# Kernel tuning notes

Measured on AMD Instinct MI355X. Metric: run time of the kernel, lower is better.

## Reference

```python
import jax, jax.numpy as jnp
import numpy as np

H = 12          # num_attention_heads
D = 64          # num_embed_hidden == attention_head_size
B, T = 4, 2048
SCALE = 1.0 / np.sqrt(D)


def setup_inputs() -> dict:
    key = jax.random.key(0)
    ks = jax.random.split(key, 7)
    P = H * D  # num_attn_proj = 768
    s = 1.0 / np.sqrt(D)
    return {
        "hidden_states": jax.random.normal(ks[0], (B, T, D), dtype=jnp.float32),
        "attention_mask": jnp.ones((B, T), dtype=jnp.float32),
        "Wq": jax.random.normal(ks[1], (D, P), dtype=jnp.float32) * s,
        "bq": jnp.zeros((P,), dtype=jnp.float32),
        "Wk": jax.random.normal(ks[2], (D, P), dtype=jnp.float32) * s,
        "bk": jnp.zeros((P,), dtype=jnp.float32),
        "Wv": jax.random.normal(ks[3], (D, P), dtype=jnp.float32) * s,
        "bv": jnp.zeros((P,), dtype=jnp.float32),
    }


def reference(hidden_states, attention_mask, Wq, bq, Wk, bk, Wv, bv):
    b, t, _ = hidden_states.shape
    # QKV projections -> [B, H, T, D]
    def proj(W, bias):
        return (hidden_states @ W + bias).reshape(b, t, H, D).transpose(0, 2, 1, 3)
    q = proj(Wq, bq)
    k = proj(Wk, bk)
    v = proj(Wv, bv)
    # [B, H, T, T] scores
    scores = jnp.einsum("bhqd,bhkd->bhqk", q, k) * SCALE
    mask = (1.0 - attention_mask)[:, None, None, :] * -10000.0
    scores = scores + mask
    attn = jax.nn.softmax(scores, axis=-1)
    # dropout is identity in eval mode
    y = jnp.einsum("bhqk,bhkd->bhqd", attn, v)
    return y.transpose(0, 2, 1, 3).reshape(b, t, H * D)
```

## Files before the change

kernel.cpp:

```cpp
#include <hip/hip_runtime.h>
#include <hip/hip_bf16.h>

#define NH 12
#define HD 64
#define NB 4
#define SEQ 2048
#define NP 768
#define LOG2E 1.44269504f
#define MASK_L2 14426.9504f

typedef __bf16 bf16x8 __attribute__((ext_vector_type(8)));
typedef __bf16 bf16x2 __attribute__((ext_vector_type(2)));
typedef float f32x2 __attribute__((ext_vector_type(2)));
typedef float f32x4 __attribute__((ext_vector_type(4)));
typedef float f32x16 __attribute__((ext_vector_type(16)));
typedef unsigned u32x4 __attribute__((ext_vector_type(4)));

static __device__ __forceinline__ bf16x8 load_bf16x8(const __bf16* p) {
    return *reinterpret_cast<const bf16x8*>(p);
}
static __device__ __forceinline__ float hw_exp2(float x) {
    return __builtin_amdgcn_exp2f(x);
}
static __device__ __forceinline__ unsigned cvtpk2(float lo, float hi) {
    f32x2 t; t[0] = lo; t[1] = hi;
    return __builtin_bit_cast(unsigned, __builtin_convertvector(t, bf16x2));
}
static __device__ __forceinline__ void async16(const __bf16* g, __bf16* l) {
    __builtin_amdgcn_global_load_lds(
        (const __attribute__((address_space(1))) unsigned*)(g),
        (__attribute__((address_space(3))) unsigned*)(l), 16, 0, 0);
}

__global__ __launch_bounds__(256) void qkv_kernel(
    const float* __restrict__ hidden,
    const float* __restrict__ Wq, const float* __restrict__ Wk,
    const float* __restrict__ Wv,
    const float* __restrict__ bq, const float* __restrict__ bk,
    const float* __restrict__ bv,
    __bf16* __restrict__ Qw, __bf16* __restrict__ Kf, __bf16* __restrict__ Vf)
{
    __shared__ __bf16 wtileT[64][72];
    __shared__ __bf16 ot[64][72];

    const int tid  = threadIdx.x;
    const int lane = tid & 63;
    const int w    = tid >> 6;
    const int g    = lane >> 4;
    const int n    = lane & 15;
    const int n32  = lane & 31;
    const int hi   = lane >> 5;

    const int row0 = blockIdx.x * 64;
    const int gi   = blockIdx.y;
    const int b_   = row0 >> 11;
    const int t0   = row0 & (SEQ - 1);
    const int kb64 = t0 >> 6;

    const float* hrow = hidden + (size_t)(row0 + w * 16 + n) * HD + 8 * g;
    f32x4 h0 = *(const f32x4*)(hrow);
    f32x4 h1 = *(const f32x4*)(hrow + 4);
    f32x4 h2 = *(const f32x4*)(hrow + 32);
    f32x4 h3 = *(const f32x4*)(hrow + 36);
    bf16x8 a0, a1;
    #pragma unroll
    for (int j = 0; j < 4; ++j) {
        a0[j]     = (__bf16)h0[j];
        a0[j + 4] = (__bf16)h1[j];
        a1[j]     = (__bf16)h2[j];
        a1[j + 4] = (__bf16)h3[j];
    }

    const int dr   = tid >> 2;
    const int coff = (tid & 3) * 16;

    for (int tt = 0; tt < 6; ++tt) {
        const int tile_id = gi * 6 + tt;
        const int proj    = tile_id / 12;
        const int head    = tile_id % 12;
        const int bh      = b_ * NH + head;
        const float* W    = proj == 0 ? Wq : (proj == 1 ? Wk : Wv);
        const float* bias = proj == 0 ? bq : (proj == 1 ? bk : bv);
        const float qs    = (proj == 0) ? 0.125f * LOG2E : 1.0f;

        const float* wr = W + (size_t)dr * NP + head * 64 + coff;
        f32x4 x0 = *(const f32x4*)(wr);
        f32x4 x1 = *(const f32x4*)(wr + 4);
        f32x4 x2 = *(const f32x4*)(wr + 8);
        f32x4 x3 = *(const f32x4*)(wr + 12);
        #pragma unroll
        for (int i = 0; i < 4; ++i) {
            wtileT[coff + i     ][dr] = (__bf16)(x0[i] * qs);
            wtileT[coff + 4 + i ][dr] = (__bf16)(x1[i] * qs);
            wtileT[coff + 8 + i ][dr] = (__bf16)(x2[i] * qs);
            wtileT[coff + 12 + i][dr] = (__bf16)(x3[i] * qs);
        }
        __syncthreads();

        #pragma unroll
        for (int dt = 0; dt < 4; ++dt) {
            const bf16x8 b0 = *(const bf16x8*)&wtileT[dt * 16 + n][8 * g];
            const bf16x8 b1 = *(const bf16x8*)&wtileT[dt * 16 + n][32 + 8 * g];
            f32x4 acc = {0.f, 0.f, 0.f, 0.f};
            acc = __builtin_amdgcn_mfma_f32_16x16x32_bf16(a0, b0, acc, 0, 0, 0);
            acc = __builtin_amdgcn_mfma_f32_16x16x32_bf16(a1, b1, acc, 0, 0, 0);
            const float bb = bias[head * 64 + dt * 16 + n] * qs;
            #pragma unroll
            for (int r = 0; r < 4; ++r)
                ot[w * 16 + 4 * g + r][dt * 16 + n] = (__bf16)(acc[r] + bb);
        }
        __syncthreads();

        if (proj == 0) {
            __bf16* dst = Qw + ((size_t)bh * SEQ + t0 + w * 16) * HD;
            const int tr = lane >> 2;
            const int d0 = (lane & 3) * 16;
            *(bf16x8*)(dst + (size_t)tr * HD + d0)     = *(const bf16x8*)&ot[w * 16 + tr][d0];
            *(bf16x8*)(dst + (size_t)tr * HD + d0 + 8) = *(const bf16x8*)&ot[w * 16 + tr][d0 + 8];
        } else if (proj == 1) {
            __bf16* base = Kf + (size_t)bh * SEQ * HD + (size_t)kb64 * 4096;
            #pragma unroll
            for (int sub = 0; sub < 2; ++sub) {
                const bf16x8 fr = *(const bf16x8*)&ot[sub * 32 + n32][w * 16 + 8 * hi];
                *(bf16x8*)(base + (size_t)(w * 2 + sub) * 512 + lane * 8) = fr;
            }
        } else {
            __bf16* base = Vf + (size_t)bh * SEQ * HD + (size_t)kb64 * 4096;
            #pragma unroll
            for (int dsub = 0; dsub < 2; ++dsub) {
                bf16x8 v;
                #pragma unroll
                for (int j = 0; j < 8; ++j)
                    v[j] = ot[w * 16 + ((j & 3) + 8 * (j >> 2) + 4 * hi)][dsub * 32 + n32];
                *(bf16x8*)(base + (size_t)(w * 2 + dsub) * 512 + lane * 8) = v;
            }
        }
    }
}

__global__ __launch_bounds__(256, 3) void flash_attn_kernel(
    const __bf16* __restrict__ Qw, const __bf16* __restrict__ Kf,
    const __bf16* __restrict__ Vf, const float* __restrict__ amask,
    float* __restrict__ out)
{
    __shared__ __align__(16) union {
        __bf16 kv[2][8192];
        float  et[4][32][68];
    } u;
    __shared__ __bf16 mdd[SEQ];

    const int tid  = threadIdx.x;
    const int lane = tid & 63;
    const int w    = tid >> 6;
    const int n32  = lane & 31;
    const int hi   = lane >> 5;

    const int bid  = blockIdx.x;
    const int xcd  = bid & 7;
    const int slot = bid >> 3;
    const int bh   = xcd * 6 + (slot >> 4);
    const int qblk = slot & 15;
    const int b_   = bh / NH;
    const int h    = bh % NH;
    const int q0   = qblk * 128 + w * 32;

    const float* mp = amask + (size_t)b_ * SEQ;
    #pragma unroll
    for (int i = 0; i < 8; ++i) {
        const int idx = w * 512 + i * 64 + lane;
        mdd[idx] = (__bf16)fmaf(mp[idx], MASK_L2, -MASK_L2);
    }

    const __bf16* Qrow = Qw + ((size_t)bh * SEQ + q0 + n32) * HD + 8 * hi;
    bf16x8 qf[4];
    #pragma unroll
    for (int d = 0; d < 4; ++d) qf[d] = load_bf16x8(Qrow + d * 16);

    bf16x8 qone;
    #pragma unroll
    for (int j = 0; j < 8; ++j) qone[j] = (__bf16)0.0f;
    if (hi == 0) qone[0] = (__bf16)1.0f;

    const size_t bhoff = (size_t)bh * SEQ * HD;
    const __bf16* gbase = (w < 2 ? Kf : Vf) + bhoff + (w & 1) * 2048 + (size_t)lane * 8;
    __bf16* const lbase = &u.kv[0][0] + ((w & 2) ? 4096 : 0) + (w & 1) * 2048;

    #pragma unroll
    for (int c = 0; c < 4; ++c) async16(gbase + c * 512, lbase + c * 512);
    __syncthreads();

    f32x16 o0 = {0,0,0,0,0,0,0,0,0,0,0,0,0,0,0,0};
    f32x16 o1 = {0,0,0,0,0,0,0,0,0,0,0,0,0,0,0,0};
    f32x2 lsl2 = {0.f, 0.f};

    for (int it = 0; it < 32; ++it) {
        const int cur = it & 1;
        const int kb  = it << 6;

        {
            const __bf16* s = gbase + (size_t)((it + 1) & 31) * 4096;
            __bf16* dl = lbase + (cur ^ 1) * 8192;
            #pragma unroll
            for (int c = 0; c < 4; ++c) async16(s + c * 512, dl + c * 512);
        }

        const __bf16* Kb = &u.kv[cur][0];
        const __bf16* Vb = Kb + 4096;

        bf16x8 kca[4], kcb[4];
        #pragma unroll
        for (int d = 0; d < 4; ++d) {
            kca[d] = load_bf16x8(Kb + (2 * d) * 512 + lane * 8);
            kcb[d] = load_bf16x8(Kb + (2 * d + 1) * 512 + lane * 8);
        }

        bf16x8 maa, mab;
        #pragma unroll
        for (int j = 0; j < 8; ++j) { maa[j] = (__bf16)0.0f; mab[j] = (__bf16)0.0f; }
        maa[0] = mdd[kb + n32];
        mab[0] = mdd[kb + 32 + n32];

        f32x16 sa = {0,0,0,0,0,0,0,0,0,0,0,0,0,0,0,0};
        f32x16 sb = {0,0,0,0,0,0,0,0,0,0,0,0,0,0,0,0};
        __builtin_amdgcn_s_setprio(1);
        #pragma unroll
        for (int d = 0; d < 4; ++d)
            sa = __builtin_amdgcn_mfma_f32_32x32x16_bf16(kca[d], qf[d], sa, 0, 0, 0);
        sa = __builtin_amdgcn_mfma_f32_32x32x16_bf16(maa, qone, sa, 0, 0, 0);
        #pragma unroll
        for (int d = 0; d < 4; ++d)
            sb = __builtin_amdgcn_mfma_f32_32x32x16_bf16(kcb[d], qf[d], sb, 0, 0, 0);
        sb = __builtin_amdgcn_mfma_f32_32x32x16_bf16(mab, qone, sb, 0, 0, 0);
        __builtin_amdgcn_s_setprio(0);

        bf16x8 vf0[4], vf1[4];
        #pragma unroll
        for (int c = 0; c < 4; ++c) {
            vf0[c] = load_bf16x8(Vb + (2 * c) * 512 + lane * 8);
            vf1[c] = load_bf16x8(Vb + (2 * c + 1) * 512 + lane * 8);
        }

        bf16x8 P0, P1;
        {
            float p[16];
            #pragma unroll
            for (int r = 0; r < 16; ++r) p[r] = hw_exp2(sa[r]);
            u32x4 B0, B1;
            #pragma unroll
            for (int i = 0; i < 4; ++i) {
                B0[i] = cvtpk2(p[2 * i],     p[2 * i + 1]);
                B1[i] = cvtpk2(p[8 + 2 * i], p[8 + 2 * i + 1]);
            }
            #pragma unroll
            for (int i = 0; i < 8; ++i) {
                f32x2 t; t[0] = p[2 * i]; t[1] = p[2 * i + 1];
                lsl2 += t;
            }
            P0 = __builtin_bit_cast(bf16x8, B0);
            P1 = __builtin_bit_cast(bf16x8, B1);
        }
        __builtin_amdgcn_s_setprio(1);
        o0 = __builtin_amdgcn_mfma_f32_32x32x16_bf16(vf0[0], P0, o0, 0, 0, 0);
        o1 = __builtin_amdgcn_mfma_f32_32x32x16_bf16(vf1[0], P0, o1, 0, 0, 0);
        o0 = __builtin_amdgcn_mfma_f32_32x32x16_bf16(vf0[1], P1, o0, 0, 0, 0);
        o1 = __builtin_amdgcn_mfma_f32_32x32x16_bf16(vf1[1], P1, o1, 0, 0, 0);
        __builtin_amdgcn_s_setprio(0);

        bf16x8 P2, P3;
        {
            float p[16];
            #pragma unroll
            for (int r = 0; r < 16; ++r) p[r] = hw_exp2(sb[r]);
            u32x4 B0, B1;
            #pragma unroll
            for (int i = 0; i < 4; ++i) {
                B0[i] = cvtpk2(p[2 * i],     p[2 * i + 1]);
                B1[i] = cvtpk2(p[8 + 2 * i], p[8 + 2 * i + 1]);
            }
            #pragma unroll
            for (int i = 0; i < 8; ++i) {
                f32x2 t; t[0] = p[2 * i]; t[1] = p[2 * i + 1];
                lsl2 += t;
            }
            P2 = __builtin_bit_cast(bf16x8, B0);
            P3 = __builtin_bit_cast(bf16x8, B1);
        }
        __builtin_amdgcn_s_setprio(1);
        o0 = __builtin_amdgcn_mfma_f32_32x32x16_bf16(vf0[2], P2, o0, 0, 0, 0);
        o1 = __builtin_amdgcn_mfma_f32_32x32x16_bf16(vf1[2], P2, o1, 0, 0, 0);
        o0 = __builtin_amdgcn_mfma_f32_32x32x16_bf16(vf0[3], P3, o0, 0, 0, 0);
        o1 = __builtin_amdgcn_mfma_f32_32x32x16_bf16(vf1[3], P3, o1, 0, 0, 0);
        __builtin_amdgcn_s_setprio(0);

        __syncthreads();
    }

    float rs = lsl2[0] + lsl2[1];
    rs += __shfl_xor(rs, 32);

    #pragma unroll
    for (int k = 0; k < 4; ++k) {
        f32x4 t0, t1;
        #pragma unroll
        for (int j = 0; j < 4; ++j) { t0[j] = o0[4 * k + j]; t1[j] = o1[4 * k + j]; }
        *(f32x4*)&u.et[w][n32][8 * k + 4 * hi]      = t0;
        *(f32x4*)&u.et[w][n32][32 + 8 * k + 4 * hi] = t1;
    }
    const int d0 = (lane & 7) * 8;
    #pragma unroll
    for (int pass = 0; pass < 4; ++pass) {
        const int q = pass * 8 + (lane >> 3);
        const float linv = 1.0f / __shfl(rs, q);
        const float* er = &u.et[w][q][d0];
        f32x4 r0 = *(const f32x4*)(er);
        f32x4 r1 = *(const f32x4*)(er + 4);
        #pragma unroll
        for (int i = 0; i < 4; ++i) { r0[i] *= linv; r1[i] *= linv; }
        float* orow = out + ((size_t)b_ * SEQ + q0 + q) * NP + h * HD + d0;
        *(f32x4*)(orow)     = r0;
        *(f32x4*)(orow + 4) = r1;
    }
}

extern "C" void kernel_launch(void* const* d_in, const int* in_sizes, int n_in,
                              void* d_out, int out_size, void* d_ws, size_t ws_size,
                              hipStream_t stream) {
    const float* hidden = (const float*)d_in[0];
    const float* amask  = (const float*)d_in[1];
    const float* Wq     = (const float*)d_in[2];
    const float* bq     = (const float*)d_in[3];
    const float* Wk     = (const float*)d_in[4];
    const float* bk     = (const float*)d_in[5];
    const float* Wv     = (const float*)d_in[6];
    const float* bv     = (const float*)d_in[7];
    float* out = (float*)d_out;

    const size_t elems = (size_t)NB * NH * SEQ * HD;
    __bf16* Qw = (__bf16*)d_ws;
    __bf16* Kf = Qw + elems;
    __bf16* Vf = Kf + elems;

    qkv_kernel<<<dim3(128, 6), 256, 0, stream>>>(
        hidden, Wq, Wk, Wv, bq, bk, bv, Qw, Kf, Vf);

    flash_attn_kernel<<<dim3(768), 256, 0, stream>>>(
        Qw, Kf, Vf, amask, out);
}
```

Baseline: 158.9 us.

## Software-pipeline QK^T of next tile with PV of previous tile using triple-buffered V

Restructures the flash-attention main loop so each iteration computes the QK^T scores for tile t while doing exp and PV for tile t-1, with K double-buffered and V triple-buffered in LDS. The loop is manually unrolled by two through a templated body, with a prologue and an epilogue for the final PV. The aim is to overlap MFMA score work with the exp/convert VALU work and V loads, hiding latency within a wave. The cost is more live accumulator registers (two sets of scores), extra LDS for the third V buffer, and more complex control flow, which could hurt occupancy at three blocks per CU.

```diff
diff --git a/kernel.cpp b/kernel.cpp
--- a/kernel.cpp
+++ b/kernel.cpp
@@ -138,15 +138,127 @@
     }
 }
 
+struct KVbuf {
+    __bf16 k[2][4096];
+    __bf16 v[3][4096];
+};
+
+union FlashLds {
+    KVbuf s;
+    float et[4][32][68];
+};
+
+static __device__ __forceinline__ int rot3(int x) { return x + 1 == 3 ? 0 : x + 1; }
+
+template<int KS, bool STG, bool DOPV>
+static __device__ __forceinline__ void fbody(
+    int t, int vprev, int vnext, int w, int lane, int n32,
+    FlashLds* u, const __bf16* mdd, const __bf16* gsrc,
+    const bf16x8 (&qf)[4], const bf16x8& qone,
+    f32x16& sap, f32x16& sbp, f32x16& san, f32x16& sbn,
+    f32x16& o0, f32x16& o1, f32x2& lsl2)
+{
+    if (STG) {
+        __bf16* dst = (w < 2) ? &u->s.k[KS ^ 1][0] + (w & 1) * 2048
+                              : &u->s.v[vnext][0] + (w & 1) * 2048;
+        const __bf16* src = gsrc + (size_t)(t + 1) * 4096;
+        #pragma unroll
+        for (int c = 0; c < 4; ++c) async16(src + c * 512, dst + c * 512);
+    }
+
+    const __bf16* Kb = &u->s.k[KS][0];
+    bf16x8 kca[4], kcb[4];
+    #pragma unroll
+    for (int d = 0; d < 4; ++d) {
+        kca[d] = load_bf16x8(Kb + (2 * d) * 512 + lane * 8);
+        kcb[d] = load_bf16x8(Kb + (2 * d + 1) * 512 + lane * 8);
+    }
+    const int kb = t << 6;
+    bf16x8 maa, mab;
+    #pragma unroll
+    for (int j = 0; j < 8; ++j) { maa[j] = (__bf16)0.0f; mab[j] = (__bf16)0.0f; }
+    maa[0] = mdd[kb + n32];
+    mab[0] = mdd[kb + 32 + n32];
+
+    f32x16 z = {0,0,0,0,0,0,0,0,0,0,0,0,0,0,0,0};
+    san = z; sbn = z;
+    __builtin_amdgcn_s_setprio(1);
+    #pragma unroll
+    for (int d = 0; d < 4; ++d)
+        san = __builtin_amdgcn_mfma_f32_32x32x16_bf16(kca[d], qf[d], san, 0, 0, 0);
+    san = __builtin_amdgcn_mfma_f32_32x32x16_bf16(maa, qone, san, 0, 0, 0);
+    #pragma unroll
+    for (int d = 0; d < 4; ++d)
+        sbn = __builtin_amdgcn_mfma_f32_32x32x16_bf16(kcb[d], qf[d], sbn, 0, 0, 0);
+    sbn = __builtin_amdgcn_mfma_f32_32x32x16_bf16(mab, qone, sbn, 0, 0, 0);
+    __builtin_amdgcn_s_setprio(0);
+
+    if (DOPV) {
+        const __bf16* Vb = &u->s.v[vprev][0];
+        bf16x8 P0, P1;
+        {
+            u32x4 B0, B1;
+            #pragma unroll
+            for (int i = 0; i < 4; ++i) {
+                float e0 = hw_exp2(sap[2 * i]),     e1 = hw_exp2(sap[2 * i + 1]);
+                float f0 = hw_exp2(sap[8 + 2 * i]), f1 = hw_exp2(sap[8 + 2 * i + 1]);
+                B0[i] = cvtpk2(e0, e1);
+                B1[i] = cvtpk2(f0, f1);
+                f32x2 acc; acc[0] = e0 + f0; acc[1] = e1 + f1;
+                lsl2 += acc;
+            }
+            P0 = __builtin_bit_cast(bf16x8, B0);
+            P1 = __builtin_bit_cast(bf16x8, B1);
+        }
+        {
+            bf16x8 v0 = load_bf16x8(Vb + 0 * 512 + lane * 8);
+            bf16x8 v1 = load_bf16x8(Vb + 1 * 512 + lane * 8);
+            bf16x8 v2 = load_bf16x8(Vb + 2 * 512 + lane * 8);
+            bf16x8 v3 = load_bf16x8(Vb + 3 * 512 + lane * 8);
+            __builtin_amdgcn_s_setprio(1);
+            o0 = __builtin_amdgcn_mfma_f32_32x32x16_bf16(v0, P0, o0, 0, 0, 0);
+            o1 = __builtin_amdgcn_mfma_f32_32x32x16_bf16(v1, P0, o1, 0, 0, 0);
+            o0 = __builtin_amdgcn_mfma_f32_32x32x16_bf16(v2, P1, o0, 0, 0, 0);
+            o1 = __builtin_amdgcn_mfma_f32_32x32x16_bf16(v3, P1, o1, 0, 0, 0);
+            __builtin_amdgcn_s_setprio(0);
+        }
+        bf16x8 P2, P3;
+        {
+            u32x4 B0, B1;
+            #pragma unroll
+            for (int i = 0; i < 4; ++i) {
+                float e0 = hw_exp2(sbp[2 * i]),     e1 = hw_exp2(sbp[2 * i + 1]);
+                float f0 = hw_exp2(sbp[8 + 2 * i]), f1 = hw_exp2(sbp[8 + 2 * i + 1]);
+                B0[i] = cvtpk2(e0, e1);
+                B1[i] = cvtpk2(f0, f1);
+                f32x2 acc; acc[0] = e0 + f0; acc[1] = e1 + f1;
+                lsl2 += acc;
+            }
+            P2 = __builtin_bit_cast(bf16x8, B0);
+            P3 = __builtin_bit_cast(bf16x8, B1);
+        }
+        {
+            bf16x8 v4 = load_bf16x8(Vb + 4 * 512 + lane * 8);
+            bf16x8 v5 = load_bf16x8(Vb + 5 * 512 + lane * 8);
+            bf16x8 v6 = load_bf16x8(Vb + 6 * 512 + lane * 8);
+            bf16x8 v7 = load_bf16x8(Vb + 7 * 512 + lane * 8);
+            __builtin_amdgcn_s_setprio(1);
+            o0 = __builtin_amdgcn_mfma_f32_32x32x16_bf16(v4, P2, o0, 0, 0, 0);
+            o1 = __builtin_amdgcn_mfma_f32_32x32x16_bf16(v5, P2, o1, 0, 0, 0);
+            o0 = __builtin_amdgcn_mfma_f32_32x32x16_bf16(v6, P3, o0, 0, 0, 0);
+            o1 = __builtin_amdgcn_mfma_f32_32x32x16_bf16(v7, P3, o1, 0, 0, 0);
+            __builtin_amdgcn_s_setprio(0);
+        }
+    }
+    __syncthreads();
+}
+
 __global__ __launch_bounds__(256, 3) void flash_attn_kernel(
     const __bf16* __restrict__ Qw, const __bf16* __restrict__ Kf,
     const __bf16* __restrict__ Vf, const float* __restrict__ amask,
     float* __restrict__ out)
 {
-    __shared__ __align__(16) union {
-        __bf16 kv[2][8192];
-        float  et[4][32][68];
-    } u;
+    __shared__ __align__(16) FlashLds u;
     __shared__ __bf16 mdd[SEQ];
 
     const int tid  = threadIdx.x;
@@ -182,121 +294,81 @@
     if (hi == 0) qone[0] = (__bf16)1.0f;
 
     const size_t bhoff = (size_t)bh * SEQ * HD;
-    const __bf16* gbase = (w < 2 ? Kf : Vf) + bhoff + (w & 1) * 2048 + (size_t)lane * 8;
-    __bf16* const lbase = &u.kv[0][0] + ((w & 2) ? 4096 : 0) + (w & 1) * 2048;
-
-    #pragma unroll
-    for (int c = 0; c < 4; ++c) async16(gbase + c * 512, lbase + c * 512);
+    const __bf16* gsrc = (w < 2 ? Kf : Vf) + bhoff + (w & 1) * 2048 + (size_t)lane * 8;
+
+    {
+        __bf16* dst = (w < 2) ? &u.s.k[0][0] + (w & 1) * 2048
+                              : &u.s.v[0][0] + (w & 1) * 2048;
+        #pragma unroll
+        for (int c = 0; c < 4; ++c) async16(gsrc + c * 512, dst + c * 512);
+    }
     __syncthreads();
 
     f32x16 o0 = {0,0,0,0,0,0,0,0,0,0,0,0,0,0,0,0};
     f32x16 o1 = {0,0,0,0,0,0,0,0,0,0,0,0,0,0,0,0};
     f32x2 lsl2 = {0.f, 0.f};
-
-    for (int it = 0; it < 32; ++it) {
-        const int cur = it & 1;
-        const int kb  = it << 6;
-
-        {
-            const __bf16* s = gbase + (size_t)((it + 1) & 31) * 4096;
-            __bf16* dl = lbase + (cur ^ 1) * 8192;
-            #pragma unroll
-            for (int c = 0; c < 4; ++c) async16(s + c * 512, dl + c * 512);
-        }
-
-        const __bf16* Kb = &u.kv[cur][0];
-        const __bf16* Vb = Kb + 4096;
-
-        bf16x8 kca[4], kcb[4];
-        #pragma unroll
-        for (int d = 0; d < 4; ++d) {
-            kca[d] = load_bf16x8(Kb + (2 * d) * 512 + lane * 8);
-            kcb[d] = load_bf16x8(Kb + (2 * d + 1) * 512 + lane * 8);
-        }
-
-        bf16x8 maa, mab;
-        #pragma unroll
-        for (int j = 0; j < 8; ++j) { maa[j] = (__bf16)0.0f; mab[j] = (__bf16)0.0f; }
-        maa[0] = mdd[kb + n32];
-        mab[0] = mdd[kb + 32 + n32];
-
-        f32x16 sa = {0,0,0,0,0,0,0,0,0,0,0,0,0,0,0,0};
-        f32x16 sb = {0,0,0,0,0,0,0,0,0,0,0,0,0,0,0,0};
-        __builtin_amdgcn_s_setprio(1);
-        #pragma unroll
-        for (int d = 0; d < 4; ++d)
-            sa = __builtin_amdgcn_mfma_f32_32x32x16_bf16(kca[d], qf[d], sa, 0, 0, 0);
-        sa = __builtin_amdgcn_mfma_f32_32x32x16_bf16(maa, qone, sa, 0, 0, 0);
-        #pragma unroll
-        for (int d = 0; d < 4; ++d)
-            sb = __builtin_amdgcn_mfma_f32_32x32x16_bf16(kcb[d], qf[d], sb, 0, 0, 0);
-        sb = __builtin_amdgcn_mfma_f32_32x32x16_bf16(mab, qone, sb, 0, 0, 0);
-        __builtin_amdgcn_s_setprio(0);
-
-        bf16x8 vf0[4], vf1[4];
-        #pragma unroll
-        for (int c = 0; c < 4; ++c) {
-            vf0[c] = load_bf16x8(Vb + (2 * c) * 512 + lane * 8);
-            vf1[c] = load_bf16x8(Vb + (2 * c + 1) * 512 + lane * 8);
-        }
-
-        bf16x8 P0, P1;
-        {
-            float p[16];
-            #pragma unroll
-            for (int r = 0; r < 16; ++r) p[r] = hw_exp2(sa[r]);
+    f32x16 saA, sbA, saB, sbB;
+
+    fbody<0, true, false>(0, 0, 1, w, lane, n32, &u, mdd, gsrc,
+                          qf, qone, saA, sbA, saA, sbA, o0, o1, lsl2);
+
+    int vprev = 0, vnext = 2;
+    #pragma unroll 1
+    for (int tp = 0; tp < 15; ++tp) {
+        const int t = 2 * tp + 1;
+        fbody<1, true, true>(t, vprev, vnext, w, lane, n32, &u, mdd, gsrc,
+                             qf, qone, saA, sbA, saB, sbB, o0, o1, lsl2);
+        vprev = rot3(vprev); vnext = rot3(vnext);
+        fbody<0, true, true>(t + 1, vprev, vnext, w, lane, n32, &u, mdd, gsrc,
+                             qf, qone, saB, sbB, saA, sbA, o0, o1, lsl2);
+        vprev = rot3(vprev); vnext = rot3(vnext);
+    }
+    fbody<1, false, true>(31, vprev, 0, w, lane, n32, &u, mdd, gsrc,
+                          qf, qone, saA, sbA, saB, sbB, o0, o1, lsl2);
+
+    {
+        const __bf16* Vb = &u.s.v[1][0];
+        bf16x8 P0, P1, P2, P3;
+        {
             u32x4 B0, B1;
             #pragma unroll
             for (int i = 0; i < 4; ++i) {
-                B0[i] = cvtpk2(p[2 * i],     p[2 * i + 1]);
-                B1[i] = cvtpk2(p[8 + 2 * i], p[8 + 2 * i + 1]);
-            }
-            #pragma unroll
-            for (int i = 0; i < 8; ++i) {
-                f32x2 t; t[0] = p[2 * i]; t[1] = p[2 * i + 1];
-                lsl2 += t;
+                float e0 = hw_exp2(saB[2 * i]),     e1 = hw_exp2(saB[2 * i + 1]);
+                float f0 = hw_exp2(saB[8 + 2 * i]), f1 = hw_exp2(saB[8 + 2 * i + 1]);
+                B0[i] = cvtpk2(e0, e1); B1[i] = cvtpk2(f0, f1);
+                f32x2 acc; acc[0] = e0 + f0; acc[1] = e1 + f1;
+                lsl2 += acc;
             }
             P0 = __builtin_bit_cast(bf16x8, B0);
             P1 = __builtin_bit_cast(bf16x8, B1);
         }
-        __builtin_amdgcn_s_setprio(1);
-        o0 = __builtin_amdgcn_mfma_f32_32x32x16_bf16(vf0[0], P0, o0, 0, 0, 0);
-        o1 = __builtin_amdgcn_mfma_f32_32x32x16_bf16(vf1[0], P0, o1, 0, 0, 0);
-        o0 = __builtin_amdgcn_mfma_f32_32x32x16_bf16(vf0[1], P1, o0, 0, 0, 0);
-        o1 = __builtin_amdgcn_mfma_f32_32x32x16_bf16(vf1[1], P1, o1, 0, 0, 0);
-        __builtin_amdgcn_s_setprio(0);
-
-        bf16x8 P2, P3;
-        {
-            float p[16];
-            #pragma unroll
-            for (int r = 0; r < 16; ++r) p[r] = hw_exp2(sb[r]);
+        {
             u32x4 B0, B1;
             #pragma unroll
             for (int i = 0; i < 4; ++i) {
-                B0[i] = cvtpk2(p[2 * i],     p[2 * i + 1]);
-                B1[i] = cvtpk2(p[8 + 2 * i], p[8 + 2 * i + 1]);
-            }
-            #pragma unroll
-            for (int i = 0; i < 8; ++i) {
-                f32x2 t; t[0] = p[2 * i]; t[1] = p[2 * i + 1];
-                lsl2 += t;
+                float e0 = hw_exp2(sbB[2 * i]),     e1 = hw_exp2(sbB[2 * i + 1]);
+                float f0 = hw_exp2(sbB[8 + 2 * i]), f1 = hw_exp2(sbB[8 + 2 * i + 1]);
+                B0[i] = cvtpk2(e0, e1); B1[i] = cvtpk2(f0, f1);
+                f32x2 acc; acc[0] = e0 + f0; acc[1] = e1 + f1;
+                lsl2 += acc;
             }
             P2 = __builtin_bit_cast(bf16x8, B0);
             P3 = __builtin_bit_cast(bf16x8, B1);
         }
-        __builtin_amdgcn_s_setprio(1);
-        o0 = __builtin_amdgcn_mfma_f32_32x32x16_bf16(vf0[2], P2, o0, 0, 0, 0);
-        o1 = __builtin_amdgcn_mfma_f32_32x32x16_bf16(vf1[2], P2, o1, 0, 0, 0);
-        o0 = __builtin_amdgcn_mfma_f32_32x32x16_bf16(vf0[3], P3, o0, 0, 0, 0);
-        o1 = __builtin_amdgcn_mfma_f32_32x32x16_bf16(vf1[3], P3, o1, 0, 0, 0);
-        __builtin_amdgcn_s_setprio(0);
-
-        __syncthreads();
+        #pragma unroll
+        for (int c = 0; c < 4; ++c) {
+            bf16x8 va = load_bf16x8(Vb + (2 * c) * 512 + lane * 8);
+            bf16x8 vb = load_bf16x8(Vb + (2 * c + 1) * 512 + lane * 8);
+            const bf16x8 P = c == 0 ? P0 : (c == 1 ? P1 : (c == 2 ? P2 : P3));
+            o0 = __builtin_amdgcn_mfma_f32_32x32x16_bf16(va, P, o0, 0, 0, 0);
+            o1 = __builtin_amdgcn_mfma_f32_32x32x16_bf16(vb, P, o1, 0, 0, 0);
+        }
     }
 
     float rs = lsl2[0] + lsl2[1];
     rs += __shfl_xor(rs, 32);
+
+    __syncthreads();
 
     #pragma unroll
     for (int k = 0; k < 4; ++k) {
```

Result: no change. 156.1 us (-1.8%).
